# Optimization experiments

Hardware: AMD Instinct MI355X
Metric: run time of the kernel (lower is better)

Reference implementation:

```python
import jax, jax.numpy as jnp
import numpy as np

POS_THRESH = 0.5
NEG_THRESH = 0.3
MIN_ANCHOR = 3
N_ANCHOR = 500000
N_GT = 200


def _iou_matrix(a, g):
    # a: [N,4], g: [M,4], boxes as (x1,y1,x2,y2)
    area_a = (a[:, 2] - a[:, 0]) * (a[:, 3] - a[:, 1])          # [N]
    area_g = (g[:, 2] - g[:, 0]) * (g[:, 3] - g[:, 1])          # [M]
    lt = jnp.maximum(a[:, None, :2], g[None, :, :2])            # [N,M,2]
    rb = jnp.minimum(a[:, None, 2:], g[None, :, 2:])            # [N,M,2]
    wh = jnp.clip(rb - lt, 0.0)
    inter = wh[..., 0] * wh[..., 1]                              # [N,M]
    return inter / (area_a[:, None] + area_g[None, :] - inter)


def _make_boxes(key, n, coord_max, size_min, size_max):
    kc, ks = jax.random.split(key)
    c = jax.random.uniform(kc, (n, 2), jnp.float32, 0.0, coord_max)
    s = jax.random.uniform(ks, (n, 2), jnp.float32, size_min, size_max)
    return jnp.concatenate([c - 0.5 * s, c + 0.5 * s], axis=1)


def setup_inputs() -> dict:
    key = jax.random.key(0)
    ka, kg = jax.random.split(key)
    anchor = _make_boxes(ka, N_ANCHOR, 1024.0, 8.0, 128.0)
    gt = _make_boxes(kg, N_GT, 1024.0, 16.0, 256.0)
    return {"anchor": anchor, "gt": gt}


def reference(anchor, gt):
    n, m = anchor.shape[0], gt.shape[0]
    iou_mat = _iou_matrix(anchor, gt)                            # [N,M]
    max_iou = jnp.max(iou_mat, axis=1)                           # [N]
    max_idx = jnp.argmax(iou_mat, axis=1).astype(jnp.int32)      # [N] (first max, like torch)
    assign = jnp.full((n,), -2, dtype=jnp.int32)
    assign = jnp.where(max_iou < NEG_THRESH, -1, assign)
    assign = jnp.where(max_iou > POS_THRESH, max_idx, assign)

    # per-GT top-k anchors (iou_mat.T : [M,N])
    vals, ranks = jax.lax.top_k(iou_mat.T, MIN_ANCHOR)           # [M,K]
    low = jnp.sum(vals > POS_THRESH, axis=1) < MIN_ANCHOR        # [M] gt lacking enough positives
    # claim[m,k]: gt m claims anchor ranks[m,k]. k==0 always (best anchor forced);
    # others only if gt is low-quality and iou > 0.1
    claim = (jnp.arange(MIN_ANCHOR)[None, :] == 0) | (low[:, None] & (vals > 0.1))
    gt_idx = jnp.broadcast_to(jnp.arange(m, dtype=jnp.int32)[:, None], (m, MIN_ANCHOR))
    claim_val = jnp.where(claim, gt_idx, -1)                     # [M,K]
    # original python loop runs gt idx in increasing order, later overwrites earlier
    # -> final winner for a contested anchor is the MAX claiming gt index: scatter-max
    forced = jnp.full((n,), -1, dtype=jnp.int32).at[ranks.reshape(-1)].max(claim_val.reshape(-1))
    assign = jnp.where(forced >= 0, forced, assign)
    return assign
```

## Files before the change

kernel.cpp:

```cpp
#include <hip/hip_runtime.h>
#include <stdint.h>


typedef unsigned int u32;
typedef unsigned short u16;
typedef unsigned long long u64;

#define POS_THRESH 0.5f
#define NEG_THRESH 0.3f
#define CLAIM_THRESH 0.1f

constexpr int NCX = 32, NCY = 32, NCELL = NCX * NCY;
constexpr float INV_CELL = 0.03125f;
constexpr float MARGIN = 64.5f;
constexpr int MPAD = 256;
constexpr int NSTRIPE = 10;
constexpr int CPAD = 16;
constexpr int HSLOTS = 1024;
constexpr int HB = 128;

#define INS3(t0, t1, t2, k) do {                                  \
    if ((k) > (t2)) {                                             \
        if ((k) > (t0))      { t2 = t1; t1 = t0; t0 = (k); }      \
        else if ((k) > (t1)) { t2 = t1; t1 = (k); }               \
        else                 { t2 = (k); }                        \
    } } while (0)

#define IOU_EVAL(a, areaA, g, areaG, inter, iou) {                \
    float ltx = fmaxf(a.x, g.x), lty = fmaxf(a.y, g.y);           \
    float rbx = fminf(a.z, g.z), rby = fminf(a.w, g.w);           \
    float ww = fmaxf(rbx - ltx, 0.0f);                            \
    float hh = fmaxf(rby - lty, 0.0f);                            \
    inter = ww * hh;                                              \
    iou = 0.0f;                                                   \
    if (inter > 0.0f) iou = inter / ((areaA + areaG) - inter);    \
}

__device__ __forceinline__ u64 shfl_xor_u64(u64 x, int mask) {
    int lo = __shfl_xor((int)(u32)x, mask, 64);
    int hi = __shfl_xor((int)(u32)(x >> 32), mask, 64);
    return ((u64)(u32)hi << 32) | (u32)lo;
}

__device__ __forceinline__ int cell_of(const float4 a) {
    float cx = 0.5f * (a.x + a.z);
    float cy = 0.5f * (a.y + a.w);
    int ix = (int)(cx * INV_CELL);
    int iy = (int)(cy * INV_CELL);
    ix = ix < 0 ? 0 : (ix > NCX - 1 ? NCX - 1 : ix);
    iy = iy < 0 ? 0 : (iy > NCY - 1 ? NCY - 1 : iy);
    return iy * NCX + ix;
}

__device__ __forceinline__ void gt_range(const float4 g, int& clx, int& chx,
                                         int& cly, int& chy) {
    clx = (int)floorf((g.x - MARGIN) * INV_CELL);
    chx = (int)floorf((g.z + MARGIN) * INV_CELL);
    cly = (int)floorf((g.y - MARGIN) * INV_CELL);
    chy = (int)floorf((g.w + MARGIN) * INV_CELL);
    clx = clx < 0 ? 0 : (clx > NCX - 1 ? NCX - 1 : clx);
    chx = chx < 0 ? 0 : (chx > NCX - 1 ? NCX - 1 : chx);
    cly = cly < 0 ? 0 : (cly > NCY - 1 ? NCY - 1 : cly);
    chy = chy < 0 ? 0 : (chy > NCY - 1 ? NCY - 1 : chy);
}

__global__ void __launch_bounds__(256) k_hist(
    const float4* __restrict__ anchor, u32* __restrict__ histPart, int N)
{
    __shared__ u32 h[NCELL];
    const int tid = threadIdx.x;
    for (int c = tid; c < NCELL; c += 256) h[c] = 0;
    __syncthreads();
    for (int i = blockIdx.x * 256 + tid; i < N; i += 256 * HB)
        atomicAdd(&h[cell_of(anchor[i])], 1u);
    __syncthreads();
    u32* mine = histPart + (size_t)blockIdx.x * NCELL;
    for (int c = tid; c < NCELL; c += 256) mine[c] = h[c];
}

__global__ void __launch_bounds__(256) k_scan(
    const u32* __restrict__ histPart, u32* __restrict__ ccPad,
    u32* __restrict__ cellStart, const float4* __restrict__ gt,
    u32* __restrict__ gtCnt, u16* __restrict__ gtIds, int M)
{
    __shared__ u32 s_sum[256];
    __shared__ u32 l_cnt[NCELL];
    const int tid = threadIdx.x;

    u32 c0 = 0, c1 = 0, c2 = 0, c3 = 0;
    for (int b = 0; b < HB; ++b) {
        const u32* p = histPart + (size_t)b * NCELL + tid * 4;
        c0 += p[0]; c1 += p[1]; c2 += p[2]; c3 += p[3];
    }
    s_sum[tid] = c0 + c1 + c2 + c3;
    for (int c = tid; c < NCELL; c += 256) l_cnt[c] = 0;
    __syncthreads();

    for (int off = 1; off < 256; off <<= 1) {
        u32 v = (tid >= off) ? s_sum[tid - off] : 0;
        __syncthreads();
        s_sum[tid] += v;
        __syncthreads();
    }

    u32 base = tid ? s_sum[tid - 1] : 0;
    cellStart[tid * 4 + 0] = base;  ccPad[(tid * 4 + 0) * CPAD] = base;
    base += c0;
    cellStart[tid * 4 + 1] = base;  ccPad[(tid * 4 + 1) * CPAD] = base;
    base += c1;
    cellStart[tid * 4 + 2] = base;  ccPad[(tid * 4 + 2) * CPAD] = base;
    base += c2;
    cellStart[tid * 4 + 3] = base;  ccPad[(tid * 4 + 3) * CPAD] = base;
    if (tid == 255) cellStart[NCELL] = s_sum[255];

    if (tid < M) {
        float4 g = gt[tid];
        int clx, chx, cly, chy;
        gt_range(g, clx, chx, cly, chy);
        for (int iy = cly; iy <= chy; ++iy)
            for (int ix = clx; ix <= chx; ++ix) {
                int c = iy * NCX + ix;
                u32 slot = atomicAdd(&l_cnt[c], 1u);
                gtIds[(size_t)c * M + slot] = (u16)tid;
            }
    }
    __syncthreads();
    for (int c = tid; c < NCELL; c += 256) gtCnt[c] = l_cnt[c];
}

__global__ void __launch_bounds__(256) k_scatass(
    const float4* __restrict__ anchor, u32* __restrict__ ccPad,
    const float4* __restrict__ gt, const u32* __restrict__ gtCnt,
    const u16* __restrict__ gtIds,
    float4* __restrict__ binnedBox, int* __restrict__ binnedIdx,
    int* __restrict__ out, int N, int M)
{
    __shared__ float4 s_g[MPAD];
    __shared__ float  s_ga[MPAD];
    const int tid = threadIdx.x;
    if (tid < M) {
        float4 g = gt[tid];
        s_g[tid]  = g;
        s_ga[tid] = (g.z - g.x) * (g.w - g.y);
    }
    __syncthreads();

    int i = blockIdx.x * 256 + tid;
    if (i >= N) return;
    float4 a = anchor[i];
    int c = cell_of(a);

    u32 pos = atomicAdd(&ccPad[c * CPAD], 1u);
    binnedBox[pos] = a;
    binnedIdx[pos] = i;

    float area_a = (a.z - a.x) * (a.w - a.y);
    int cnt = (int)gtCnt[c];
    const u16* list = gtIds + (size_t)c * M;

    u64 best = 0;
    for (int k = 0; k < cnt; ++k) {
        int m = list[k];
        float4 g = s_g[m];
        float inter, iou;
        IOU_EVAL(a, area_a, g, s_ga[m], inter, iou);
        if (inter > 0.0f) {
            u64 key = ((u64)__float_as_uint(iou) << 32) | (~(u32)m);
            best = key > best ? key : best;
        }
    }
    u32 ib = (u32)(best >> 32);
    int v = -2;
    if (ib < __float_as_uint(NEG_THRESH)) v = -1;
    if (ib > __float_as_uint(POS_THRESH)) v = (int)(~(u32)best);
    out[i] = v;
}

__global__ void __launch_bounds__(256) k_top3(
    const float4* __restrict__ binnedBox, const int* __restrict__ binnedIdx,
    const float4* __restrict__ gt, const u32* __restrict__ cellStart,
    u64* __restrict__ partial3, int M)
{
    const int s    = blockIdx.x;
    const int m    = blockIdx.y;
    const int tid  = threadIdx.x;
    const int lane = tid & 63;
    const int w    = tid >> 6;

    float4 g = gt[m];
    float area_g = (g.z - g.x) * (g.w - g.y);
    int clx, chx, cly, chy;
    gt_range(g, clx, chx, cly, chy);

    u64 t0 = 0x00000000FFFFFFFFULL;
    u64 t1 = 0x00000000FFFFFFFEULL;
    u64 t2 = 0x00000000FFFFFFFDULL;

    int q = 0;
    for (int iy = cly; iy <= chy; ++iy)
        for (int ix = clx; ix <= chx; ++ix, ++q) {
            if (q % NSTRIPE != s) continue;
            int c = iy * NCX + ix;
            int cs = (int)cellStart[c];
            int ce = (int)cellStart[c + 1];
            for (int p = cs + tid; p < ce; p += 256) {
                float4 a = binnedBox[p];
                int  idx = binnedIdx[p];
                float area_a = (a.z - a.x) * (a.w - a.y);
                float inter, iou;
                IOU_EVAL(a, area_a, g, area_g, inter, iou);
                if (inter > 0.0f) {
                    u64 key = ((u64)__float_as_uint(iou) << 32) | (~(u32)idx);
                    INS3(t0, t1, t2, key);
                }
            }
        }

    for (int off = 1; off < 64; off <<= 1) {
        u64 o0 = shfl_xor_u64(t0, off);
        u64 o1 = shfl_xor_u64(t1, off);
        u64 o2 = shfl_xor_u64(t2, off);
        INS3(t0, t1, t2, o0);
        INS3(t0, t1, t2, o1);
        INS3(t0, t1, t2, o2);
    }

    __shared__ u64 s_red[4][3];
    if (lane == 0) { s_red[w][0] = t0; s_red[w][1] = t1; s_red[w][2] = t2; }
    __syncthreads();
    if (tid == 0) {
        u64 q0 = 0, q1 = 0, q2 = 0;
        for (int wv = 0; wv < 4; ++wv) {
            INS3(q0, q1, q2, s_red[wv][0]);
            INS3(q0, q1, q2, s_red[wv][1]);
            INS3(q0, q1, q2, s_red[wv][2]);
        }
        size_t b = ((size_t)m * NSTRIPE + s) * 3;
        partial3[b + 0] = q0;
        partial3[b + 1] = q1;
        partial3[b + 2] = q2;
    }
}

__global__ void __launch_bounds__(256) k_claims(
    const u64* __restrict__ partial3, int* __restrict__ out, int M)
{
    __shared__ u64 s_key[3 * MPAD];
    __shared__ u64 h_val[HSLOTS];
    __shared__ u32 h_tag[HSLOTS];
    const int tid = threadIdx.x;

    for (int i = tid; i < HSLOTS; i += 256) { h_val[i] = 0; h_tag[i] = 0; }

    if (tid < M) {
        u64 q0 = 0, q1 = 0, q2 = 0;
        const u64* p = partial3 + (size_t)tid * NSTRIPE * 3;
        for (int c = 0; c < NSTRIPE * 3; ++c) INS3(q0, q1, q2, p[c]);

        float v0 = __uint_as_float((u32)(q0 >> 32));
        float v1 = __uint_as_float((u32)(q1 >> 32));
        float v2 = __uint_as_float((u32)(q2 >> 32));
        u32 a0 = ~(u32)q0;
        u32 a1 = ~(u32)q1;
        u32 a2 = ~(u32)q2;

        int npos = (v0 > POS_THRESH) + (v1 > POS_THRESH) + (v2 > POS_THRESH);
        bool low = npos < 3;

        s_key[tid * 3 + 0] = ((u64)a0 << 32) | (u32)(tid + 1);
        s_key[tid * 3 + 1] = (low && v1 > CLAIM_THRESH)
            ? (((u64)a1 << 32) | (u32)(tid + 1)) : 0ULL;
        s_key[tid * 3 + 2] = (low && v2 > CLAIM_THRESH)
            ? (((u64)a2 << 32) | (u32)(tid + 1)) : 0ULL;
    }
    __syncthreads();

    const int tote = 3 * M;
    for (int e = tid; e < tote; e += 256) {
        u64 my = s_key[e];
        if (my == 0) continue;
        u32 myA = (u32)(my >> 32);
        u32 slot = (myA * 2654435761u) & (HSLOTS - 1);
        while (true) {
            u32 prev = atomicCAS(&h_tag[slot], 0u, myA + 1u);
            if (prev == 0u || prev == myA + 1u) {
                atomicMax(&h_val[slot], my);
                break;
            }
            slot = (slot + 1) & (HSLOTS - 1);
        }
    }
    __syncthreads();
    for (int e = tid; e < tote; e += 256) {
        u64 my = s_key[e];
        if (my == 0) continue;
        u32 myA = (u32)(my >> 32);
        u32 slot = (myA * 2654435761u) & (HSLOTS - 1);
        while (h_tag[slot] != myA + 1u) slot = (slot + 1) & (HSLOTS - 1);
        if (h_val[slot] == my) out[myA] = (int)(my & 0xffffffffULL) - 1;
    }
}

extern "C" void kernel_launch(void* const* d_in, const int* in_sizes, int n_in,
                              void* d_out, int out_size, void* d_ws, size_t ws_size,
                              hipStream_t stream) {
    const float4* anchor = (const float4*)d_in[0];
    const float4* gt     = (const float4*)d_in[1];
    int N = in_sizes[0] / 4;
    int M = in_sizes[1] / 4;
    int* out = (int*)d_out;

    char* ws = (char*)d_ws;
    size_t off = 0;
    auto alloc = [&](size_t bytes, size_t align) -> void* {
        off = (off + align - 1) / align * align;
        void* p = ws + off;
        off += bytes;
        return p;
    };
    u32* histPart   = (u32*)alloc((size_t)HB * NCELL * 4, 64);
    u32* ccPad      = (u32*)alloc((size_t)NCELL * CPAD * 4, 64);
    u32* cellStart  = (u32*)alloc((NCELL + 1) * 4, 4);
    u32* gtCnt      = (u32*)alloc(NCELL * 4, 4);
    u64* partial3   = (u64*)alloc((size_t)M * NSTRIPE * 3 * 8, 8);
    u16* gtIds      = (u16*)alloc((size_t)NCELL * M * 2, 2);
    float4* binnedBox = (float4*)alloc((size_t)N * 16, 16);
    int* binnedIdx    = (int*)alloc((size_t)N * 4, 4);

    int nb = (N + 255) / 256;
    k_hist<<<HB, 256, 0, stream>>>(anchor, histPart, N);
    k_scan<<<1, 256, 0, stream>>>(histPart, ccPad, cellStart, gt, gtCnt,
                                  gtIds, M);
    k_scatass<<<nb, 256, 0, stream>>>(anchor, ccPad, gt, gtCnt, gtIds,
                                      binnedBox, binnedIdx, out, N, M);
    k_top3<<<dim3(NSTRIPE, M), 256, 0, stream>>>(binnedBox, binnedIdx, gt,
                                                 cellStart, partial3, M);
    k_claims<<<1, 256, 0, stream>>>(partial3, out, M);
}
```

Before: 121.0 us.

## Fuse per-GT top-3 into anchor pass via shared-memory atomic cascade

```diff
diff --git a/kernel.cpp b/kernel.cpp
--- a/kernel.cpp
+++ b/kernel.cpp
@@ -14,17 +14,8 @@
 constexpr float INV_CELL = 0.03125f;
 constexpr float MARGIN = 64.5f;
 constexpr int MPAD = 256;
-constexpr int NSTRIPE = 10;
-constexpr int CPAD = 16;
 constexpr int HSLOTS = 1024;
-constexpr int HB = 128;
-
-#define INS3(t0, t1, t2, k) do {                                  \
-    if ((k) > (t2)) {                                             \
-        if ((k) > (t0))      { t2 = t1; t1 = t0; t0 = (k); }      \
-        else if ((k) > (t1)) { t2 = t1; t1 = (k); }               \
-        else                 { t2 = (k); }                        \
-    } } while (0)
+constexpr int GRID_MAIN = 1024;
 
 #define IOU_EVAL(a, areaA, g, areaG, inter, iou) {                \
     float ltx = fmaxf(a.x, g.x), lty = fmaxf(a.y, g.y);           \
@@ -34,12 +25,6 @@
     inter = ww * hh;                                              \
     iou = 0.0f;                                                   \
     if (inter > 0.0f) iou = inter / ((areaA + areaG) - inter);    \
-}
-
-__device__ __forceinline__ u64 shfl_xor_u64(u64 x, int mask) {
-    int lo = __shfl_xor((int)(u32)x, mask, 64);
-    int hi = __shfl_xor((int)(u32)(x >> 32), mask, 64);
-    return ((u64)(u32)hi << 32) | (u32)lo;
 }
 
 __device__ __forceinline__ int cell_of(const float4 a) {
@@ -64,54 +49,21 @@
     chy = chy < 0 ? 0 : (chy > NCY - 1 ? NCY - 1 : chy);
 }
 
-__global__ void __launch_bounds__(256) k_hist(
-    const float4* __restrict__ anchor, u32* __restrict__ histPart, int N)
+#define CASCADE3(p0, p1, p2, key) {                               \
+    u64 x_ = (key);                                               \
+    u64 o_ = atomicMax(&(p0), x_); x_ = o_ < x_ ? o_ : x_;        \
+    o_ = atomicMax(&(p1), x_); x_ = o_ < x_ ? o_ : x_;            \
+    atomicMax(&(p2), x_);                                         \
+}
+
+__global__ void __launch_bounds__(256) k_prep(
+    const float4* __restrict__ gt, u32* __restrict__ gtCnt,
+    u16* __restrict__ gtIds, u64* __restrict__ final3, int M)
 {
-    __shared__ u32 h[NCELL];
-    const int tid = threadIdx.x;
-    for (int c = tid; c < NCELL; c += 256) h[c] = 0;
-    __syncthreads();
-    for (int i = blockIdx.x * 256 + tid; i < N; i += 256 * HB)
-        atomicAdd(&h[cell_of(anchor[i])], 1u);
-    __syncthreads();
-    u32* mine = histPart + (size_t)blockIdx.x * NCELL;
-    for (int c = tid; c < NCELL; c += 256) mine[c] = h[c];
-}
-
-__global__ void __launch_bounds__(256) k_scan(
-    const u32* __restrict__ histPart, u32* __restrict__ ccPad,
-    u32* __restrict__ cellStart, const float4* __restrict__ gt,
-    u32* __restrict__ gtCnt, u16* __restrict__ gtIds, int M)
-{
-    __shared__ u32 s_sum[256];
     __shared__ u32 l_cnt[NCELL];
     const int tid = threadIdx.x;
-
-    u32 c0 = 0, c1 = 0, c2 = 0, c3 = 0;
-    for (int b = 0; b < HB; ++b) {
-        const u32* p = histPart + (size_t)b * NCELL + tid * 4;
-        c0 += p[0]; c1 += p[1]; c2 += p[2]; c3 += p[3];
-    }
-    s_sum[tid] = c0 + c1 + c2 + c3;
     for (int c = tid; c < NCELL; c += 256) l_cnt[c] = 0;
     __syncthreads();
-
-    for (int off = 1; off < 256; off <<= 1) {
-        u32 v = (tid >= off) ? s_sum[tid - off] : 0;
-        __syncthreads();
-        s_sum[tid] += v;
-        __syncthreads();
-    }
-
-    u32 base = tid ? s_sum[tid - 1] : 0;
-    cellStart[tid * 4 + 0] = base;  ccPad[(tid * 4 + 0) * CPAD] = base;
-    base += c0;
-    cellStart[tid * 4 + 1] = base;  ccPad[(tid * 4 + 1) * CPAD] = base;
-    base += c1;
-    cellStart[tid * 4 + 2] = base;  ccPad[(tid * 4 + 2) * CPAD] = base;
-    base += c2;
-    cellStart[tid * 4 + 3] = base;  ccPad[(tid * 4 + 3) * CPAD] = base;
-    if (tid == 255) cellStart[NCELL] = s_sum[255];
 
     if (tid < M) {
         float4 g = gt[tid];
@@ -123,127 +75,75 @@
                 u32 slot = atomicAdd(&l_cnt[c], 1u);
                 gtIds[(size_t)c * M + slot] = (u16)tid;
             }
+        final3[tid * 3 + 0] = 0x00000000FFFFFFFFULL;
+        final3[tid * 3 + 1] = 0x00000000FFFFFFFEULL;
+        final3[tid * 3 + 2] = 0x00000000FFFFFFFDULL;
     }
     __syncthreads();
     for (int c = tid; c < NCELL; c += 256) gtCnt[c] = l_cnt[c];
 }
 
-__global__ void __launch_bounds__(256) k_scatass(
-    const float4* __restrict__ anchor, u32* __restrict__ ccPad,
-    const float4* __restrict__ gt, const u32* __restrict__ gtCnt,
-    const u16* __restrict__ gtIds,
-    float4* __restrict__ binnedBox, int* __restrict__ binnedIdx,
-    int* __restrict__ out, int N, int M)
+__global__ void __launch_bounds__(256) k_main(
+    const float4* __restrict__ anchor, const float4* __restrict__ gt,
+    const u32* __restrict__ gtCnt, const u16* __restrict__ gtIds,
+    u64* __restrict__ final3, int* __restrict__ out, int N, int M)
 {
     __shared__ float4 s_g[MPAD];
     __shared__ float  s_ga[MPAD];
+    __shared__ u64    tbl[3 * MPAD];
     const int tid = threadIdx.x;
+
     if (tid < M) {
         float4 g = gt[tid];
         s_g[tid]  = g;
         s_ga[tid] = (g.z - g.x) * (g.w - g.y);
     }
-    __syncthreads();
-
-    int i = blockIdx.x * 256 + tid;
-    if (i >= N) return;
-    float4 a = anchor[i];
-    int c = cell_of(a);
-
-    u32 pos = atomicAdd(&ccPad[c * CPAD], 1u);
-    binnedBox[pos] = a;
-    binnedIdx[pos] = i;
-
-    float area_a = (a.z - a.x) * (a.w - a.y);
-    int cnt = (int)gtCnt[c];
-    const u16* list = gtIds + (size_t)c * M;
-
-    u64 best = 0;
-    for (int k = 0; k < cnt; ++k) {
-        int m = list[k];
-        float4 g = s_g[m];
-        float inter, iou;
-        IOU_EVAL(a, area_a, g, s_ga[m], inter, iou);
-        if (inter > 0.0f) {
-            u64 key = ((u64)__float_as_uint(iou) << 32) | (~(u32)m);
-            best = key > best ? key : best;
-        }
-    }
-    u32 ib = (u32)(best >> 32);
-    int v = -2;
-    if (ib < __float_as_uint(NEG_THRESH)) v = -1;
-    if (ib > __float_as_uint(POS_THRESH)) v = (int)(~(u32)best);
-    out[i] = v;
-}
-
-__global__ void __launch_bounds__(256) k_top3(
-    const float4* __restrict__ binnedBox, const int* __restrict__ binnedIdx,
-    const float4* __restrict__ gt, const u32* __restrict__ cellStart,
-    u64* __restrict__ partial3, int M)
-{
-    const int s    = blockIdx.x;
-    const int m    = blockIdx.y;
-    const int tid  = threadIdx.x;
-    const int lane = tid & 63;
-    const int w    = tid >> 6;
-
-    float4 g = gt[m];
-    float area_g = (g.z - g.x) * (g.w - g.y);
-    int clx, chx, cly, chy;
-    gt_range(g, clx, chx, cly, chy);
-
-    u64 t0 = 0x00000000FFFFFFFFULL;
-    u64 t1 = 0x00000000FFFFFFFEULL;
-    u64 t2 = 0x00000000FFFFFFFDULL;
-
-    int q = 0;
-    for (int iy = cly; iy <= chy; ++iy)
-        for (int ix = clx; ix <= chx; ++ix, ++q) {
-            if (q % NSTRIPE != s) continue;
-            int c = iy * NCX + ix;
-            int cs = (int)cellStart[c];
-            int ce = (int)cellStart[c + 1];
-            for (int p = cs + tid; p < ce; p += 256) {
-                float4 a = binnedBox[p];
-                int  idx = binnedIdx[p];
-                float area_a = (a.z - a.x) * (a.w - a.y);
-                float inter, iou;
-                IOU_EVAL(a, area_a, g, area_g, inter, iou);
-                if (inter > 0.0f) {
-                    u64 key = ((u64)__float_as_uint(iou) << 32) | (~(u32)idx);
-                    INS3(t0, t1, t2, key);
-                }
+    for (int e = tid; e < 3 * MPAD; e += 256) tbl[e] = 0;
+    __syncthreads();
+
+    for (int i = blockIdx.x * 256 + tid; i < N; i += 256 * GRID_MAIN) {
+        float4 a = anchor[i];
+        float area_a = (a.z - a.x) * (a.w - a.y);
+        int c   = cell_of(a);
+        int cnt = (int)gtCnt[c];
+        const u16* list = gtIds + (size_t)c * M;
+        u32 nai = ~(u32)i;
+
+        u64 best = 0;
+        for (int k = 0; k < cnt; ++k) {
+            int m = list[k];
+            float4 g = s_g[m];
+            float inter, iou;
+            IOU_EVAL(a, area_a, g, s_ga[m], inter, iou);
+            if (inter > 0.0f) {
+                u32 ib = __float_as_uint(iou);
+                u64 kb = ((u64)ib << 32) | (~(u32)m);
+                best = kb > best ? kb : best;
+                u64 kt = ((u64)ib << 32) | nai;
+                if (kt > tbl[m * 3 + 2])
+                    CASCADE3(tbl[m * 3 + 0], tbl[m * 3 + 1], tbl[m * 3 + 2], kt);
             }
         }
-
-    for (int off = 1; off < 64; off <<= 1) {
-        u64 o0 = shfl_xor_u64(t0, off);
-        u64 o1 = shfl_xor_u64(t1, off);
-        u64 o2 = shfl_xor_u64(t2, off);
-        INS3(t0, t1, t2, o0);
-        INS3(t0, t1, t2, o1);
-        INS3(t0, t1, t2, o2);
-    }
-
-    __shared__ u64 s_red[4][3];
-    if (lane == 0) { s_red[w][0] = t0; s_red[w][1] = t1; s_red[w][2] = t2; }
-    __syncthreads();
-    if (tid == 0) {
-        u64 q0 = 0, q1 = 0, q2 = 0;
-        for (int wv = 0; wv < 4; ++wv) {
-            INS3(q0, q1, q2, s_red[wv][0]);
-            INS3(q0, q1, q2, s_red[wv][1]);
-            INS3(q0, q1, q2, s_red[wv][2]);
-        }
-        size_t b = ((size_t)m * NSTRIPE + s) * 3;
-        partial3[b + 0] = q0;
-        partial3[b + 1] = q1;
-        partial3[b + 2] = q2;
+        u32 ib = (u32)(best >> 32);
+        int v = -2;
+        if (ib < __float_as_uint(NEG_THRESH)) v = -1;
+        if (ib > __float_as_uint(POS_THRESH)) v = (int)(~(u32)best);
+        out[i] = v;
+    }
+    __syncthreads();
+
+    for (int e = tid; e < 3 * M; e += 256) {
+        u64 v = tbl[e];
+        if ((u32)(v >> 32) == 0) continue;
+        int m = e / 3;
+        u64* g3 = final3 + m * 3;
+        if (v <= g3[2]) continue;
+        CASCADE3(g3[0], g3[1], g3[2], v);
     }
 }
 
 __global__ void __launch_bounds__(256) k_claims(
-    const u64* __restrict__ partial3, int* __restrict__ out, int M)
+    const u64* __restrict__ final3, int* __restrict__ out, int M)
 {
     __shared__ u64 s_key[3 * MPAD];
     __shared__ u64 h_val[HSLOTS];
@@ -253,9 +153,9 @@
     for (int i = tid; i < HSLOTS; i += 256) { h_val[i] = 0; h_tag[i] = 0; }
 
     if (tid < M) {
-        u64 q0 = 0, q1 = 0, q2 = 0;
-        const u64* p = partial3 + (size_t)tid * NSTRIPE * 3;
-        for (int c = 0; c < NSTRIPE * 3; ++c) INS3(q0, q1, q2, p[c]);
+        u64 q0 = final3[tid * 3 + 0];
+        u64 q1 = final3[tid * 3 + 1];
+        u64 q2 = final3[tid * 3 + 2];
 
         float v0 = __uint_as_float((u32)(q0 >> 32));
         float v1 = __uint_as_float((u32)(q1 >> 32));
@@ -318,22 +218,12 @@
         off += bytes;
         return p;
     };
-    u32* histPart   = (u32*)alloc((size_t)HB * NCELL * 4, 64);
-    u32* ccPad      = (u32*)alloc((size_t)NCELL * CPAD * 4, 64);
-    u32* cellStart  = (u32*)alloc((NCELL + 1) * 4, 4);
-    u32* gtCnt      = (u32*)alloc(NCELL * 4, 4);
-    u64* partial3   = (u64*)alloc((size_t)M * NSTRIPE * 3 * 8, 8);
-    u16* gtIds      = (u16*)alloc((size_t)NCELL * M * 2, 2);
-    float4* binnedBox = (float4*)alloc((size_t)N * 16, 16);
-    int* binnedIdx    = (int*)alloc((size_t)N * 4, 4);
-
-    int nb = (N + 255) / 256;
-    k_hist<<<HB, 256, 0, stream>>>(anchor, histPart, N);
-    k_scan<<<1, 256, 0, stream>>>(histPart, ccPad, cellStart, gt, gtCnt,
-                                  gtIds, M);
-    k_scatass<<<nb, 256, 0, stream>>>(anchor, ccPad, gt, gtCnt, gtIds,
-                                      binnedBox, binnedIdx, out, N, M);
-    k_top3<<<dim3(NSTRIPE, M), 256, 0, stream>>>(binnedBox, binnedIdx, gt,
-                                                 cellStart, partial3, M);
-    k_claims<<<1, 256, 0, stream>>>(partial3, out, M);
-}
+    u32* gtCnt  = (u32*)alloc(NCELL * 4, 64);
+    u64* final3 = (u64*)alloc((size_t)MPAD * 3 * 8, 64);
+    u16* gtIds  = (u16*)alloc((size_t)NCELL * M * 2, 2);
+
+    k_prep<<<1, 256, 0, stream>>>(gt, gtCnt, gtIds, final3, M);
+    k_main<<<GRID_MAIN, 256, 0, stream>>>(anchor, gt, gtCnt, gtIds,
+                                          final3, out, N, M);
+    k_claims<<<1, 256, 0, stream>>>(final3, out, M);
+}
```

Result: slower. 123.6 us (+2.1%).
